# Kernel tuning notes

Hardware: AMD Instinct MI355X
Metric: run time of the kernel (lower is better)

## Reference

```python
import jax, jax.numpy as jnp
import numpy as np


def setup_inputs() -> dict:
    key = jax.random.key(0)
    ks = jax.random.split(key, 10)
    B, T = 1024, 8192
    # X features: [time, current I, temperature T, voltage U]
    t = jnp.cumsum(jax.random.uniform(ks[0], (B, T, 1), jnp.float32) + 0.5, axis=1)  # increasing time
    feats = jax.random.normal(ks[1], (B, T, 3), jnp.float32)
    X = jnp.concatenate([t, feats], axis=-1)  # [B, T, 4]
    # SC: [Q (capacity), eta_0, R, SOC_init_base]; keep Q away from 0
    SC = jax.random.uniform(ks[2], (B, 4), jnp.float32, minval=0.5, maxval=1.5)
    std = 0.1
    # SOC_init_net: Linear(4,1) -> Softplus -> Linear(1,1), normal(0,0.1) weights, zero bias
    W1i = jax.random.normal(ks[3], (1, 4), jnp.float32) * std
    b1i = jnp.zeros((1,), jnp.float32)
    W2i = jax.random.normal(ks[4], (1, 1), jnp.float32) * std
    b2i = jnp.zeros((1,), jnp.float32)
    # eta_net: Linear(2,1) -> Softplus -> Linear(1,1)
    W1e = jax.random.normal(ks[5], (1, 2), jnp.float32) * std
    b1e = jnp.zeros((1,), jnp.float32)
    W2e = jax.random.normal(ks[6], (1, 1), jnp.float32) * std
    b2e = jnp.zeros((1,), jnp.float32)
    return {"X": X, "SC": SC, "W1i": W1i, "b1i": b1i, "W2i": W2i, "b2i": b2i,
            "W1e": W1e, "b1e": b1e, "W2e": W2e, "b2e": b2e}


def reference(X, SC, W1i, b1i, W2i, b2i, W1e, b1e, W2e, b2e):
    # X: [B, T, 4] = (t, I, Temp, U); SC: [B, 4] = (Q, eta_0, R, soc_base)
    I = X[..., 1:2]      # [B, T, 1]
    Temp = X[..., 2:3]   # [B, T, 1]
    U = X[..., 3:4]      # [B, T, 1]
    R = SC[..., 2:3]     # [B, 1]
    # SOC_init_net on first-timestep features
    feat0 = jnp.concatenate([I[:, 0, :], Temp[:, 0, :], U[:, 0, :], R], axis=-1)  # [B, 4]
    h0 = jax.nn.softplus(feat0 @ W1i.T + b1i)
    soc_net = h0 @ W2i.T + b2i                     # [B, 1]
    SOC_init = SC[..., 3:4] * (1.0 + soc_net)      # [B, 1]
    # eta_net over all timesteps
    feat = jnp.concatenate([I, Temp], axis=-1)     # [B, T, 2]
    h = jax.nn.softplus(feat @ W1e.T + b1e)
    delta_eta = h @ W2e.T + b2e                    # [B, T, 1]
    # ODE RHS: dSOC/dt = eta_0 * (1 + delta_eta) * I / (3600 * Q)
    Q = SC[..., 0:1][:, None, :]                   # [B, 1, 1]
    eta0 = SC[..., 1:2][:, None, :]                # [B, 1, 1]
    f = eta0 * (1.0 + delta_eta) * I / (3600.0 * Q)  # [B, T, 1]
    # Euler integration: y_{k+1} = y_k + (t_{k+1} - t_k) * f(x_k, y_k); f independent of y -> cumsum
    ts = X[..., 0:1]                               # [B, T, 1]
    dt = ts[:, 1:] - ts[:, :-1]                    # [B, T-1, 1]
    incr = dt * f[:, :-1]                          # [B, T-1, 1]
    zero = jnp.zeros_like(SOC_init)[:, None, :]    # [B, 1, 1]
    SOC = SOC_init[:, None, :] + jnp.concatenate([zero, jnp.cumsum(incr, axis=1)], axis=1)
    return SOC                                     # [B, T, 1]
```

## Files before the change

kernel.cpp:

```cpp
#include <hip/hip_runtime.h>
#include <type_traits>


static __device__ __forceinline__ float bf2f(unsigned int u) {
    union { unsigned int i; float f; } v;
    v.i = u << 16;
    return v.f;
}
static __device__ __forceinline__ unsigned short f2bf(float f) {
    union { unsigned int i; float f; } v;
    v.f = f;
    unsigned int x = v.i;
    return (unsigned short)((x + 0x7fffu + ((x >> 16) & 1u)) >> 16);
}
static __device__ __forceinline__ float sp_fast(float x) {
    return __logf(1.f + __expf(x));
}

struct F4 { float ts, I, Te, U; };
static __device__ __forceinline__ F4 dec(ushort4 x) {
    return {bf2f(x.x), bf2f(x.y), bf2f(x.z), bf2f(x.w)};
}
static __device__ __forceinline__ F4 dec(float4 x) {
    return {x.x, x.y, x.z, x.w};
}

template <bool BF16>
static __device__ __forceinline__ float ld(const void* p, int i) {
    return BF16 ? bf2f(((const unsigned short*)p)[i]) : ((const float*)p)[i];
}

constexpr int BLOCK = 256;

template <int NCH>
static __device__ void scan_k4(
    const float* __restrict__ X, const float* __restrict__ SC,
    const float* __restrict__ W1i, const float* __restrict__ b1i,
    const float* __restrict__ W2i, const float* __restrict__ b2i,
    const float* __restrict__ W1e, const float* __restrict__ b1e,
    const float* __restrict__ W2e, const float* __restrict__ b2e,
    float* __restrict__ outv, float* s_wtot, float* s_init)
{
    constexpr int SPAN = NCH * 256;
    constexpr int T    = SPAN * 4;

    const int b    = blockIdx.x;
    const int tid  = threadIdx.x;
    const int lane = tid & 63;
    const int wave = tid >> 6;
    const int ws   = wave * SPAN;

    const float Q    = SC[b * 4 + 0];
    const float eta0 = SC[b * 4 + 1];
    const float R    = SC[b * 4 + 2];
    const float S3   = SC[b * 4 + 3];
    const float w1e0 = W1e[0];
    const float w1e1 = W1e[1];
    const float vb1e = b1e[0];
    const float coef = eta0 / (3600.f * Q);
    const float c2   = coef * W2e[0];
    const float c1   = coef * (1.f + b2e[0]);

    const float4* Xrow = (const float4*)X + (size_t)b * T;

    float4 ring[8];
    #pragma unroll
    for (int c = 0; c < 2; ++c)
        #pragma unroll
        for (int j = 0; j < 4; ++j)
            ring[c * 4 + j] = Xrow[ws + c * 256 + lane * 4 + j];

    float ts_c, f_c;
    if (wave > 0) {
        const float4 vp = Xrow[ws - 1];
        const float hp = sp_fast(fmaf(vp.y, w1e0, fmaf(vp.z, w1e1, vb1e)));
        f_c  = fmaf(c2, hp, c1) * vp.y;
        ts_c = vp.x;
    } else {
        const float4 v0 = Xrow[0];
        ts_c = v0.x;
        f_c  = 0.f;
        const float pre = fmaf(v0.y, W1i[0],
                          fmaf(v0.z, W1i[1],
                          fmaf(v0.w, W1i[2],
                          fmaf(R, W1i[3], b1i[0]))));
        const float h0 = sp_fast(pre);
        if (lane == 0)
            *s_init = S3 * (1.f + fmaf(h0, W2i[0], b2i[0]));
    }

    float vals[NCH * 4];
    float carry = 0.f;
    #pragma unroll
    for (int c = 0; c < NCH; ++c) {
        const int s = (c & 1) * 4;
        const float4 v0 = ring[s + 0];
        const float4 v1 = ring[s + 1];
        const float4 v2 = ring[s + 2];
        const float4 v3 = ring[s + 3];
        if (c + 2 < NCH) {
            #pragma unroll
            for (int j = 0; j < 4; ++j)
                ring[s + j] = Xrow[ws + (c + 2) * 256 + lane * 4 + j];
        }

        const float f0 = fmaf(c2, sp_fast(fmaf(v0.y, w1e0, fmaf(v0.z, w1e1, vb1e))), c1) * v0.y;
        const float f1 = fmaf(c2, sp_fast(fmaf(v1.y, w1e0, fmaf(v1.z, w1e1, vb1e))), c1) * v1.y;
        const float f2 = fmaf(c2, sp_fast(fmaf(v2.y, w1e0, fmaf(v2.z, w1e1, vb1e))), c1) * v2.y;
        const float f3 = fmaf(c2, sp_fast(fmaf(v3.y, w1e0, fmaf(v3.z, w1e1, vb1e))), c1) * v3.y;

        float pts = __shfl_up(v3.x, 1, 64);
        float pf  = __shfl_up(f3,   1, 64);
        if (lane == 0) { pts = ts_c; pf = f_c; }

        const float g0 = (v0.x - pts) * pf;
        const float g1 = fmaf(v1.x - v0.x, f0, g0);
        const float g2 = fmaf(v2.x - v1.x, f1, g1);
        const float g3 = fmaf(v3.x - v2.x, f2, g2);

        float S = g3;
        #pragma unroll
        for (int d = 1; d < 64; d <<= 1) {
            const float u = __shfl_up(S, d, 64);
            if (lane >= d) S += u;
        }
        const float tb = carry + (S - g3);
        vals[c * 4 + 0] = g0 + tb;
        vals[c * 4 + 1] = g1 + tb;
        vals[c * 4 + 2] = g2 + tb;
        vals[c * 4 + 3] = g3 + tb;

        carry += __shfl(S, 63, 64);
        ts_c   = __shfl(v3.x, 63, 64);
        f_c    = __shfl(f3, 63, 64);
    }
    if (lane == 0) s_wtot[wave] = carry;
    __syncthreads();

    float base = *s_init;
    #pragma unroll
    for (int w = 0; w < 3; ++w)
        if (w < wave) base += s_wtot[w];

    float4* orow = (float4*)(outv + (size_t)b * T);
    #pragma unroll
    for (int c = 0; c < NCH; ++c) {
        float4 o;
        o.x = vals[c * 4 + 0] + base;
        o.y = vals[c * 4 + 1] + base;
        o.z = vals[c * 4 + 2] + base;
        o.w = vals[c * 4 + 3] + base;
        orow[wave * (SPAN / 4) + c * 64 + lane] = o;
    }
}

__global__ __launch_bounds__(BLOCK, 4) void socnet_reg(
    const void* __restrict__ X, const void* __restrict__ SC,
    const void* __restrict__ W1i, const void* __restrict__ b1i,
    const void* __restrict__ W2i, const void* __restrict__ b2i,
    const void* __restrict__ W1e, const void* __restrict__ b1e,
    const void* __restrict__ W2e, const void* __restrict__ b2e,
    void* __restrict__ out)
{
    __shared__ float s_wtot[4];
    __shared__ float s_init;
    scan_k4<8>((const float*)X, (const float*)SC,
               (const float*)W1i, (const float*)b1i,
               (const float*)W2i, (const float*)b2i,
               (const float*)W1e, (const float*)b1e,
               (const float*)W2e, (const float*)b2e,
               (float*)out, s_wtot, &s_init);
}

template <bool BF16>
static __device__ void scan_serial(
    const void* __restrict__ Xv, const void* __restrict__ SCv,
    const void* __restrict__ W1i, const void* __restrict__ b1i,
    const void* __restrict__ W2i, const void* __restrict__ b2i,
    const void* __restrict__ W1e, const void* __restrict__ b1e,
    const void* __restrict__ W2e, const void* __restrict__ b2e,
    void* __restrict__ outv, int T,
    float* s_wts, float* s_wf, float* s_wsum, float* s_carr)
{
    using XVec = typename std::conditional<BF16, ushort4, float4>::type;
    const int b = blockIdx.x, tid = threadIdx.x;
    const int lane = tid & 63, wave = tid >> 6;
    const int ntile = (T + BLOCK - 1) / BLOCK;

    const float Q    = ld<BF16>(SCv, b * 4 + 0);
    const float eta0 = ld<BF16>(SCv, b * 4 + 1);
    const float R    = ld<BF16>(SCv, b * 4 + 2);
    const float S3   = ld<BF16>(SCv, b * 4 + 3);
    const float w1e0 = ld<BF16>(W1e, 0);
    const float w1e1 = ld<BF16>(W1e, 1);
    const float vb1e = ld<BF16>(b1e, 0);
    const float coef = eta0 / (3600.f * Q);
    const float c2   = coef * ld<BF16>(W2e, 0);
    const float c1   = coef * (1.f + ld<BF16>(b2e, 0));

    const XVec* Xrow = (const XVec*)Xv + (size_t)b * T;

    for (int tile = 0; tile < ntile; ++tile) {
        const int t = tile * BLOCK + tid;
        const bool act = t < T;
        F4 v = {0.f, 0.f, 0.f, 0.f};
        if (act) v = dec(Xrow[t]);
        const float f = fmaf(c2, sp_fast(fmaf(v.I, w1e0, fmaf(v.Te, w1e1, vb1e))), c1) * v.I;

        float pts = __shfl_up(v.ts, 1, 64);
        float pf  = __shfl_up(f, 1, 64);

        __syncthreads();
        if (lane == 63) { s_wts[wave] = v.ts; s_wf[wave] = f; }
        if (tile == 0 && tid == 0) {
            const float pre = fmaf(v.I, ld<BF16>(W1i, 0),
                              fmaf(v.Te, ld<BF16>(W1i, 1),
                              fmaf(v.U, ld<BF16>(W1i, 2),
                              fmaf(R, ld<BF16>(W1i, 3), ld<BF16>(b1i, 0)))));
            s_carr[0] = S3 * (1.f + fmaf(sp_fast(pre), ld<BF16>(W2i, 0), ld<BF16>(b2i, 0)));
        }
        __syncthreads();
        if (lane == 0) {
            if (wave == 0) { if (tile > 0) { pts = s_carr[1]; pf = s_carr[2]; } }
            else { pts = s_wts[wave - 1]; pf = s_wf[wave - 1]; }
        }
        float g = (t == 0 || !act) ? 0.f : (v.ts - pts) * pf;
        #pragma unroll
        for (int d = 1; d < 64; d <<= 1) {
            const float u = __shfl_up(g, d, 64);
            if (lane >= d) g += u;
        }
        if (lane == 63) s_wsum[wave] = g;
        __syncthreads();
        float soc = s_carr[0];
        #pragma unroll
        for (int w = 0; w < 3; ++w) if (w < wave) soc += s_wsum[w];
        soc += g;
        if (act) {
            if (BF16) ((unsigned short*)outv)[(size_t)b * T + t] = f2bf(soc);
            else      ((float*)outv)[(size_t)b * T + t] = soc;
        }
        __syncthreads();
        if (tid == BLOCK - 1) { s_carr[0] = soc; s_carr[1] = v.ts; s_carr[2] = f; }
    }
}

__global__ __launch_bounds__(BLOCK) void socnet_serial_k(
    const void* __restrict__ X, const void* __restrict__ SC,
    const void* __restrict__ W1i, const void* __restrict__ b1i,
    const void* __restrict__ W2i, const void* __restrict__ b2i,
    const void* __restrict__ W1e, const void* __restrict__ b1e,
    const void* __restrict__ W2e, const void* __restrict__ b2e,
    void* __restrict__ out, int T)
{
    __shared__ float s_wts[4], s_wf[4], s_wsum[4], s_carr[3];
    const unsigned int* scw = (const unsigned int*)SC;
    const float l0 = bf2f(scw[0] & 0xFFFFu), l1 = bf2f(scw[1] & 0xFFFFu);
    const float l2 = bf2f(scw[2] & 0xFFFFu), l3 = bf2f(scw[3] & 0xFFFFu);
    const bool isbf =
        (l0 >= 0.45f && l0 <= 1.55f) && (l1 >= 0.45f && l1 <= 1.55f) &&
        (l2 >= 0.45f && l2 <= 1.55f) && (l3 >= 0.45f && l3 <= 1.55f);
    if (isbf) scan_serial<true >(X, SC, W1i, b1i, W2i, b2i, W1e, b1e, W2e, b2e,
                                 out, T, s_wts, s_wf, s_wsum, s_carr);
    else      scan_serial<false>(X, SC, W1i, b1i, W2i, b2i, W1e, b1e, W2e, b2e,
                                 out, T, s_wts, s_wf, s_wsum, s_carr);
}

extern "C" void kernel_launch(void* const* d_in, const int* in_sizes, int n_in,
                              void* d_out, int out_size, void* d_ws, size_t ws_size,
                              hipStream_t stream) {
    const int B = in_sizes[1] / 4;
    const int T = in_sizes[0] / (B * 4);

    if (T == 8192) {
        socnet_reg<<<dim3(B), dim3(BLOCK), 0, stream>>>(
            d_in[0], d_in[1], d_in[2], d_in[3], d_in[4], d_in[5],
            d_in[6], d_in[7], d_in[8], d_in[9], d_out);
    } else {
        socnet_serial_k<<<dim3(B), dim3(BLOCK), 0, stream>>>(
            d_in[0], d_in[1], d_in[2], d_in[3], d_in[4], d_in[5],
            d_in[6], d_in[7], d_in[8], d_in[9], d_out, T);
    }
}
```

Before: 215.0 us.

## Replace per-wave register scan with 512-thread tiled block scan

The T=8192 path now uses 512-thread blocks that walk the row in four tiles of 2048 timesteps. Each tile does a per-thread 4-element scan, a wave shuffle scan, and a cross-wave combine through double-buffered shared memory, then writes its output right away. This replaces the old scheme of 4 waves each holding 8 chunks in registers with ring-buffer prefetch, so register pressure drops and occupancy can rise. The cost is one __syncthreads per tile, the loss of the explicit prefetch pipelining, and an extra boundary load per wave per tile.

```diff
diff --git a/kernel.cpp b/kernel.cpp
--- a/kernel.cpp
+++ b/kernel.cpp
@@ -30,30 +30,35 @@
     return BF16 ? bf2f(((const unsigned short*)p)[i]) : ((const float*)p)[i];
 }
 
-constexpr int BLOCK = 256;
-
-template <int NCH>
-static __device__ void scan_k4(
-    const float* __restrict__ X, const float* __restrict__ SC,
-    const float* __restrict__ W1i, const float* __restrict__ b1i,
-    const float* __restrict__ W2i, const float* __restrict__ b2i,
-    const float* __restrict__ W1e, const float* __restrict__ b1e,
-    const float* __restrict__ W2e, const float* __restrict__ b2e,
-    float* __restrict__ outv, float* s_wtot, float* s_init)
+constexpr int BLOCK  = 256;
+constexpr int TBLOCK = 512;
+
+__global__ __launch_bounds__(TBLOCK, 8) void socnet_tile(
+    const void* __restrict__ Xv, const void* __restrict__ SCv,
+    const void* __restrict__ W1iv, const void* __restrict__ b1iv,
+    const void* __restrict__ W2iv, const void* __restrict__ b2iv,
+    const void* __restrict__ W1ev, const void* __restrict__ b1ev,
+    const void* __restrict__ W2ev, const void* __restrict__ b2ev,
+    void* __restrict__ outv)
 {
-    constexpr int SPAN = NCH * 256;
-    constexpr int T    = SPAN * 4;
+    const float* X   = (const float*)Xv;
+    const float* SC  = (const float*)SCv;
+    const float* W1i = (const float*)W1iv;
+    const float* b1i = (const float*)b1iv;
+    const float* W2i = (const float*)W2iv;
+    const float* b2i = (const float*)b2iv;
+    const float* W1e = (const float*)W1ev;
+    const float* b1e = (const float*)b1ev;
+    const float* W2e = (const float*)W2ev;
+    const float* b2e = (const float*)b2ev;
 
     const int b    = blockIdx.x;
     const int tid  = threadIdx.x;
     const int lane = tid & 63;
     const int wave = tid >> 6;
-    const int ws   = wave * SPAN;
 
     const float Q    = SC[b * 4 + 0];
     const float eta0 = SC[b * 4 + 1];
-    const float R    = SC[b * 4 + 2];
-    const float S3   = SC[b * 4 + 3];
     const float w1e0 = W1e[0];
     const float w1e1 = W1e[1];
     const float vb1e = b1e[0];
@@ -61,47 +66,31 @@
     const float c2   = coef * W2e[0];
     const float c1   = coef * (1.f + b2e[0]);
 
-    const float4* Xrow = (const float4*)X + (size_t)b * T;
-
-    float4 ring[8];
-    #pragma unroll
-    for (int c = 0; c < 2; ++c)
-        #pragma unroll
-        for (int j = 0; j < 4; ++j)
-            ring[c * 4 + j] = Xrow[ws + c * 256 + lane * 4 + j];
-
-    float ts_c, f_c;
-    if (wave > 0) {
-        const float4 vp = Xrow[ws - 1];
-        const float hp = sp_fast(fmaf(vp.y, w1e0, fmaf(vp.z, w1e1, vb1e)));
-        f_c  = fmaf(c2, hp, c1) * vp.y;
-        ts_c = vp.x;
-    } else {
-        const float4 v0 = Xrow[0];
-        ts_c = v0.x;
-        f_c  = 0.f;
-        const float pre = fmaf(v0.y, W1i[0],
-                          fmaf(v0.z, W1i[1],
-                          fmaf(v0.w, W1i[2],
-                          fmaf(R, W1i[3], b1i[0]))));
-        const float h0 = sp_fast(pre);
-        if (lane == 0)
-            *s_init = S3 * (1.f + fmaf(h0, W2i[0], b2i[0]));
-    }
-
-    float vals[NCH * 4];
+    const float4* Xrow = (const float4*)X + (size_t)b * 8192;
+    float4*       orow = (float4*)outv + (size_t)b * 2048;
+
+    __shared__ float s_wt[2][8];
+    __shared__ float s_init;
+
     float carry = 0.f;
     #pragma unroll
-    for (int c = 0; c < NCH; ++c) {
-        const int s = (c & 1) * 4;
-        const float4 v0 = ring[s + 0];
-        const float4 v1 = ring[s + 1];
-        const float4 v2 = ring[s + 2];
-        const float4 v3 = ring[s + 3];
-        if (c + 2 < NCH) {
-            #pragma unroll
-            for (int j = 0; j < 4; ++j)
-                ring[s + j] = Xrow[ws + (c + 2) * 256 + lane * 4 + j];
+    for (int tile = 0; tile < 4; ++tile) {
+        const int tbase = tile * 2048;
+        const int e0    = tbase + tid * 4;
+
+        const float4 v0 = Xrow[e0 + 0];
+        const float4 v1 = Xrow[e0 + 1];
+        const float4 v2 = Xrow[e0 + 2];
+        const float4 v3 = Xrow[e0 + 3];
+
+        float ts_c, f_c;
+        if (tile == 0 && wave == 0) {
+            ts_c = v0.x;
+            f_c  = 0.f;
+        } else {
+            const float4 vp = Xrow[tbase + wave * 256 - 1];
+            ts_c = vp.x;
+            f_c  = fmaf(c2, sp_fast(fmaf(vp.y, w1e0, fmaf(vp.z, w1e1, vb1e))), c1) * vp.y;
         }
 
         const float f0 = fmaf(c2, sp_fast(fmaf(v0.y, w1e0, fmaf(v0.z, w1e1, vb1e))), c1) * v0.y;
@@ -124,52 +113,38 @@
             const float u = __shfl_up(S, d, 64);
             if (lane >= d) S += u;
         }
-        const float tb = carry + (S - g3);
-        vals[c * 4 + 0] = g0 + tb;
-        vals[c * 4 + 1] = g1 + tb;
-        vals[c * 4 + 2] = g2 + tb;
-        vals[c * 4 + 3] = g3 + tb;
-
-        carry += __shfl(S, 63, 64);
-        ts_c   = __shfl(v3.x, 63, 64);
-        f_c    = __shfl(f3, 63, 64);
+
+        if (lane == 63) s_wt[tile & 1][wave] = S;
+        if (tile == 0 && tid == 0) {
+            const float pre = fmaf(v0.y, W1i[0],
+                              fmaf(v0.z, W1i[1],
+                              fmaf(v0.w, W1i[2],
+                              fmaf(SC[b * 4 + 2], W1i[3], b1i[0]))));
+            s_init = SC[b * 4 + 3] *
+                     (1.f + fmaf(sp_fast(pre), W2i[0], b2i[0]));
+        }
+        __syncthreads();
+
+        if (tile == 0) carry = s_init;
+
+        float add = carry + (S - g3);
+        #pragma unroll
+        for (int w = 0; w < 7; ++w)
+            if (w < wave) add += s_wt[tile & 1][w];
+
+        float4 o;
+        o.x = g0 + add;
+        o.y = g1 + add;
+        o.z = g2 + add;
+        o.w = g3 + add;
+        orow[tile * 512 + tid] = o;
+
+        float wsum = 0.f;
+        #pragma unroll
+        for (int w = 0; w < 8; ++w)
+            wsum += s_wt[tile & 1][w];
+        carry += wsum;
     }
-    if (lane == 0) s_wtot[wave] = carry;
-    __syncthreads();
-
-    float base = *s_init;
-    #pragma unroll
-    for (int w = 0; w < 3; ++w)
-        if (w < wave) base += s_wtot[w];
-
-    float4* orow = (float4*)(outv + (size_t)b * T);
-    #pragma unroll
-    for (int c = 0; c < NCH; ++c) {
-        float4 o;
-        o.x = vals[c * 4 + 0] + base;
-        o.y = vals[c * 4 + 1] + base;
-        o.z = vals[c * 4 + 2] + base;
-        o.w = vals[c * 4 + 3] + base;
-        orow[wave * (SPAN / 4) + c * 64 + lane] = o;
-    }
-}
-
-__global__ __launch_bounds__(BLOCK, 4) void socnet_reg(
-    const void* __restrict__ X, const void* __restrict__ SC,
-    const void* __restrict__ W1i, const void* __restrict__ b1i,
-    const void* __restrict__ W2i, const void* __restrict__ b2i,
-    const void* __restrict__ W1e, const void* __restrict__ b1e,
-    const void* __restrict__ W2e, const void* __restrict__ b2e,
-    void* __restrict__ out)
-{
-    __shared__ float s_wtot[4];
-    __shared__ float s_init;
-    scan_k4<8>((const float*)X, (const float*)SC,
-               (const float*)W1i, (const float*)b1i,
-               (const float*)W2i, (const float*)b2i,
-               (const float*)W1e, (const float*)b1e,
-               (const float*)W2e, (const float*)b2e,
-               (float*)out, s_wtot, &s_init);
 }
 
 template <bool BF16>
@@ -273,7 +248,7 @@
     const int T = in_sizes[0] / (B * 4);
 
     if (T == 8192) {
-        socnet_reg<<<dim3(B), dim3(BLOCK), 0, stream>>>(
+        socnet_tile<<<dim3(B), dim3(TBLOCK), 0, stream>>>(
             d_in[0], d_in[1], d_in[2], d_in[3], d_in[4], d_in[5],
             d_in[6], d_in[7], d_in[8], d_in[9], d_out);
     } else {
```

New measurement: 218.2 us. No clear change (+1.4%).
